# Performance work log

Measured on AMD Instinct MI355X. Metric: run time of the kernel, lower is better.

## Reference

```python
import jax, jax.numpy as jnp
import numpy as np

B, S, H = 2, 2048, 2048
NH = 16
Q_LORA = 1536
KV_LORA = 512
NOPE = 128
ROPE = 64
QHD = NOPE + ROPE  # 192
VHD = 128
FF = 8192
EPS = 1e-6
THETA = 10000.0


def rmsnorm(x, w, eps=EPS):
    var = jnp.mean(jnp.square(x), axis=-1, keepdims=True)
    return w * (x * jax.lax.rsqrt(var + eps))


def rotate_half(x):
    x1 = x[..., : x.shape[-1] // 2]
    x2 = x[..., x.shape[-1] // 2 :]
    return jnp.concatenate((-x2, x1), axis=-1)


def _deinterleave(x):
    # torch: x.view(b,h,s,d//2,2).transpose(0,1,2,4,3).reshape(b,h,s,d)
    b, h, s, d = x.shape
    return x.reshape(b, h, s, d // 2, 2).transpose(0, 1, 2, 4, 3).reshape(b, h, s, d)


def setup_inputs() -> dict:
    key = jax.random.key(0)
    ks = jax.random.split(key, 16)
    sc = 0.02
    # RoPE tables [S, ROPE]
    inv_freq = 1.0 / (THETA ** (np.arange(0, ROPE, 2, dtype=np.float64) / ROPE))
    freqs = np.outer(np.arange(S, dtype=np.float64), inv_freq)
    emb = np.concatenate([freqs, freqs], axis=-1)
    pos = jnp.sort(jax.random.randint(ks[15], (B, S), 0, S), axis=-1)
    return {
        "hidden_states": jax.random.normal(ks[0], (B, S, H), jnp.float32),
        "ln1_w": jnp.ones((H,), jnp.float32),
        "q_a_kernel": jax.random.normal(ks[1], (H, Q_LORA), jnp.float32) * sc,
        "q_a_ln_w": jnp.ones((Q_LORA,), jnp.float32),
        "q_b_kernel": jax.random.normal(ks[2], (Q_LORA, NH * QHD), jnp.float32) * sc,
        "kv_a_kernel": jax.random.normal(ks[3], (H, KV_LORA + ROPE), jnp.float32) * sc,
        "kv_a_ln_w": jnp.ones((KV_LORA,), jnp.float32),
        "kv_b_kernel": jax.random.normal(ks[4], (KV_LORA, NH * (NOPE + VHD)), jnp.float32) * sc,
        "o_kernel": jax.random.normal(ks[5], (NH * VHD, H), jnp.float32) * sc,
        "ln2_w": jnp.ones((H,), jnp.float32),
        "gate_kernel": jax.random.normal(ks[6], (H, FF), jnp.float32) * sc,
        "up_kernel": jax.random.normal(ks[7], (H, FF), jnp.float32) * sc,
        "down_kernel": jax.random.normal(ks[8], (FF, H), jnp.float32) * sc,
        "sin": jnp.asarray(np.sin(emb), jnp.float32),
        "cos": jnp.asarray(np.cos(emb), jnp.float32),
        "position_ids": pos,
    }


def reference(hidden_states, ln1_w, q_a_kernel, q_a_ln_w, q_b_kernel,
              kv_a_kernel, kv_a_ln_w, kv_b_kernel, o_kernel, ln2_w,
              gate_kernel, up_kernel, down_kernel, sin, cos, position_ids):
    b, s, h = hidden_states.shape
    x = rmsnorm(hidden_states, ln1_w)

    # --- MLA attention ---
    q = rmsnorm(x @ q_a_kernel, q_a_ln_w) @ q_b_kernel        # [b,s,NH*QHD]
    q = q.reshape(b, s, NH, QHD).transpose(0, 2, 1, 3)        # [b,NH,s,QHD]
    q_nope, q_pe = q[..., :NOPE], q[..., NOPE:]

    ckv = x @ kv_a_kernel                                     # [b,s,KV_LORA+ROPE]
    k_pe = ckv[..., KV_LORA:].reshape(b, s, 1, ROPE).transpose(0, 2, 1, 3)  # [b,1,s,ROPE]
    kv = rmsnorm(ckv[..., :KV_LORA], kv_a_ln_w) @ kv_b_kernel
    kv = kv.reshape(b, s, NH, NOPE + VHD).transpose(0, 2, 1, 3)
    k_nope = kv[..., :NOPE]
    v = kv[..., NOPE:]                                        # [b,NH,s,VHD]

    cos_e = cos[position_ids][:, None]                        # [b,1,s,ROPE]
    sin_e = sin[position_ids][:, None]
    q_pe = _deinterleave(q_pe)
    k_pe = _deinterleave(k_pe)
    q_pe = q_pe * cos_e + rotate_half(q_pe) * sin_e
    k_pe = k_pe * cos_e + rotate_half(k_pe) * sin_e

    qs = jnp.concatenate([q_nope, q_pe], axis=-1)             # [b,NH,s,QHD]
    ks = jnp.concatenate([k_nope, jnp.broadcast_to(k_pe, (b, NH, s, ROPE))], axis=-1)

    scale = QHD ** -0.5
    scores = jnp.einsum("bhqd,bhkd->bhqk", qs, ks) * scale
    causal = jnp.tril(jnp.ones((s, s), dtype=bool))
    scores = jnp.where(causal, scores, jnp.finfo(scores.dtype).min)
    probs = jax.nn.softmax(scores, axis=-1)
    attn = jnp.einsum("bhqk,bhkd->bhqd", probs, v)            # [b,NH,s,VHD]
    attn = attn.transpose(0, 2, 1, 3).reshape(b, s, NH * VHD)
    attn_out = attn @ o_kernel

    h1 = hidden_states + attn_out

    # --- dense MLP (SwiGLU) ---
    x2 = rmsnorm(h1, ln2_w)
    mlp = (jax.nn.silu(x2 @ gate_kernel) * (x2 @ up_kernel)) @ down_kernel
    return h1 + mlp
```

## Files before the change

### kernel.cpp

```cpp
#include <hip/hip_runtime.h>
#include <hip/hip_bf16.h>
#include <cstdint>

#define B_ 2
#define S_ 2048
#define H_ 2048
#define NH_ 16
#define QL_ 1536
#define KVL_ 512
#define NOPE_ 128
#define ROPE_ 64
#define QHD_ 192
#define VHD_ 128
#define FF_ 8192
#define BS_ (B_ * S_)
#define CKVP_ 640
#define KVW_ (NOPE_ + VHD_)

typedef __hip_bfloat16 bf16;
typedef __attribute__((ext_vector_type(8))) short short8_t;
typedef __attribute__((ext_vector_type(4))) float f32x4;

__device__ __forceinline__ float ldf(const float* p, size_t i) { return p[i]; }
__device__ __forceinline__ float ldf(const bf16* p, size_t i) { return __bfloat162float(p[i]); }
__device__ __forceinline__ void stf(float* p, size_t i, float v) { p[i] = v; }
__device__ __forceinline__ void stf(bf16* p, size_t i, float v) { p[i] = __float2bfloat16(v); }

__device__ __forceinline__ void gload16(const void* g, void* l)
{
    __builtin_amdgcn_global_load_lds((const unsigned int*)g, (unsigned int*)l, 16, 0, 0);
}

__global__ __launch_bounds__(256) void transp_bf16(
    const float* __restrict__ in, bf16* __restrict__ out, int K, int N, int Npad)
{
    __shared__ float t[32][33];
    const int n0 = blockIdx.x * 32, k0 = blockIdx.y * 32;
    for (int r = threadIdx.y; r < 32; r += 8) {
        const int n = n0 + threadIdx.x;
        t[r][threadIdx.x] = (n < N) ? in[(size_t)(k0 + r) * N + n] : 0.f;
    }
    __syncthreads();
    for (int r = threadIdx.y; r < 32; r += 8) {
        out[(size_t)(n0 + r) * K + k0 + threadIdx.x] = __float2bfloat16(t[threadIdx.x][r]);
    }
}

template<typename InT, typename OutT>
__global__ __launch_bounds__(256) void rmsnorm2(
    const InT* __restrict__ in, const float* __restrict__ w,
    OutT* __restrict__ out, int cols, int istride, int ostride)
{
    const int row = blockIdx.x;
    const InT* ip = in + (size_t)row * istride;
    OutT* op = out + (size_t)row * ostride;

    float ss = 0.f;
    for (int c = threadIdx.x; c < cols; c += 256) {
        float v = ldf(ip, c);
        ss = fmaf(v, v, ss);
    }
    #pragma unroll
    for (int off = 32; off; off >>= 1) ss += __shfl_xor(ss, off);
    __shared__ float red[4];
    if ((threadIdx.x & 63) == 0) red[threadIdx.x >> 6] = ss;
    __syncthreads();
    const float total = red[0] + red[1] + red[2] + red[3];
    const float scale = rsqrtf(total / (float)cols + 1e-6f);
    for (int c = threadIdx.x; c < cols; c += 256) {
        stf(op, c, ldf(ip, c) * scale * w[c]);
    }
}

template<int MODE, typename OutT>
__global__ __launch_bounds__(256) void gemm_bf16(
    const bf16* __restrict__ A, const bf16* __restrict__ BT,
    const float* __restrict__ Df, const bf16* __restrict__ Db,
    OutT* __restrict__ C, int M, int N, int K)
{
    __shared__ short As[128 * 32];
    __shared__ short Bs[128 * 32];
    const int tid = threadIdx.x;
    const int wid = tid >> 6, lane = tid & 63;
    const int bm = blockIdx.y * 128, bn = blockIdx.x * 128;
    const int wr = (wid >> 1) * 64, wc = (wid & 1) * 64;
    const int l16 = lane & 15;
    const int lk = (lane >> 4) << 3;

    f32x4 acc[4][4] = {};

    for (int k0 = 0; k0 < K; k0 += 32) {
        #pragma unroll
        for (int is = 0; is < 2; ++is) {
            const int c = is * 256 + tid;
            const int row = c >> 2;
            const int cb = (c & 3) * 16;
            const char* srcA = (const char*)A + ((size_t)(bm + row) * K + k0) * 2 + cb;
            const char* srcB = (const char*)BT + ((size_t)(bn + row) * K + k0) * 2 + cb;
            char* dstA = (char*)As + (is * 256 + wid * 64) * 16;
            char* dstB = (char*)Bs + (is * 256 + wid * 64) * 16;
            gload16(srcA, dstA);
            gload16(srcB, dstB);
        }
        __syncthreads();

        short8_t a[4], b[4];
        const short* ApW = As + (wr + l16) * 32 + lk;
        const short* BpW = Bs + (wc + l16) * 32 + lk;
        #pragma unroll
        for (int m = 0; m < 4; ++m) a[m] = *(const short8_t*)(ApW + m * 16 * 32);
        #pragma unroll
        for (int n = 0; n < 4; ++n) b[n] = *(const short8_t*)(BpW + n * 16 * 32);
        #pragma unroll
        for (int m = 0; m < 4; ++m)
            #pragma unroll
            for (int n = 0; n < 4; ++n)
                acc[m][n] = __builtin_amdgcn_mfma_f32_16x16x32_bf16(a[m], b[n], acc[m][n], 0, 0, 0);
        __syncthreads();
    }

    const int r0 = bm + wr + ((lane >> 4) << 2);
    const int c0 = bn + wc + l16;
    #pragma unroll
    for (int m = 0; m < 4; ++m) {
        #pragma unroll
        for (int n = 0; n < 4; ++n) {
            const int row = r0 + m * 16;
            const int col = c0 + n * 16;
            #pragma unroll
            for (int r = 0; r < 4; ++r) {
                const size_t off = (size_t)(row + r) * N + col;
                float v = acc[m][n][r];
                if (MODE == 1) v += Df[off];
                if (MODE == 2) {
                    const float g = __bfloat162float(Db[off]);
                    v *= g / (1.f + __expf(-g));
                }
                stf(C, off, v);
            }
        }
    }
}

template<int MODE, typename OutT>
__device__ __forceinline__ void epi_store(
    OutT* __restrict__ C, const float* __restrict__ Df, const bf16* __restrict__ Db,
    int N, int row, int col, float v)
{
    const size_t off = (size_t)row * N + col;
    if (MODE == 1) v += Df[off];
    if (MODE == 2) {
        const float g = __bfloat162float(Db[off]);
        v *= g / (1.f + __expf(-g));
    }
    stf(C, off, v);
}

__device__ __forceinline__ short8_t ldsfrag(const short* half_base, int r, int c)
{
    return *(const short8_t*)(half_base + r * 64 + ((c ^ (r & 7)) << 3));
}

template<int MODE, typename OutT>
__global__ __launch_bounds__(512, 2) void gemm256(
    const bf16* __restrict__ A, const bf16* __restrict__ BT,
    const float* __restrict__ Df, const bf16* __restrict__ Db,
    OutT* __restrict__ C, int M, int N, int K)
{
    __shared__ short lds[2][2][2][128 * 64];

    const int tid = threadIdx.x;
    const int wid = tid >> 6, lane = tid & 63;
    const int wm = wid >> 2, wn = wid & 3;
    const int l16 = lane & 15, hk = lane >> 4;

    const int nwg = gridDim.x * gridDim.y;
    const int orig = blockIdx.y * gridDim.x + blockIdx.x;
    const int q = nwg >> 3, r8 = nwg & 7;
    const int xcd = orig & 7, lid = orig >> 3;
    const int wg = (xcd < r8 ? xcd * (q + 1) : r8 * (q + 1) + (xcd - r8) * q) + lid;
    const int bn = (wg % gridDim.x) * 256;
    const int bm = (wg / gridDim.x) * 256;

    f32x4 acc[8][4] = {};
    const int nt = K >> 6;

    auto stage_half = [&](const bf16* gbase, short* lbase) {
        #pragma unroll
        for (int i = 0; i < 2; ++i) {
            const int ch = i * 512 + tid;
            const int row = ch >> 3, pc = ch & 7;
            const int gc = pc ^ (row & 7);
            const char* src = (const char*)(gbase + (size_t)row * K + gc * 8);
            char* dst = (char*)lbase + (i * 512 + wid * 64) * 16;
            gload16(src, dst);
        }
    };
    auto stage_tile = [&](int t, int buf) {
        const int k0 = t << 6;
        stage_half(A + (size_t)bm * K + k0,          &lds[buf][0][0][0]);
        stage_half(A + (size_t)(bm + 128) * K + k0,  &lds[buf][0][1][0]);
        stage_half(BT + (size_t)bn * K + k0,         &lds[buf][1][0][0]);
        stage_half(BT + (size_t)(bn + 128) * K + k0, &lds[buf][1][1][0]);
    };

    stage_tile(0, 0);
    stage_tile(1, 1);
    asm volatile("s_waitcnt vmcnt(8)" ::: "memory");
    __builtin_amdgcn_s_barrier();

    int cur = 0;
    for (int t = 0; t < nt; ++t) {
        const short* Ah = &lds[cur][0][wm][0];
        const short* Bh = &lds[cur][1][wn >> 1][0];
        const int brr = (wn & 1) * 64;

        short8_t bfr[4][2], afr[2][2];

        #pragma unroll
        for (int nf = 0; nf < 4; ++nf)
            #pragma unroll
            for (int ks = 0; ks < 2; ++ks)
                bfr[nf][ks] = ldsfrag(Bh, brr + nf * 16 + l16, ks * 4 + hk);
        #pragma unroll
        for (int mi = 0; mi < 2; ++mi)
            #pragma unroll
            for (int ks = 0; ks < 2; ++ks)
                afr[mi][ks] = ldsfrag(Ah, mi * 16 + l16, ks * 4 + hk);
        __builtin_amdgcn_s_barrier();
        __builtin_amdgcn_s_setprio(1);
        #pragma unroll
        for (int mi = 0; mi < 2; ++mi)
            #pragma unroll
            for (int nf = 0; nf < 4; ++nf)
                #pragma unroll
                for (int ks = 0; ks < 2; ++ks)
                    acc[mi][nf] = __builtin_amdgcn_mfma_f32_16x16x32_bf16(
                        afr[mi][ks], bfr[nf][ks], acc[mi][nf], 0, 0, 0);
        __builtin_amdgcn_s_setprio(0);
        __builtin_amdgcn_s_barrier();

        #pragma unroll
        for (int ph = 1; ph < 4; ++ph) {
            #pragma unroll
            for (int mi = 0; mi < 2; ++mi)
                #pragma unroll
                for (int ks = 0; ks < 2; ++ks)
                    afr[mi][ks] = ldsfrag(Ah, ph * 32 + mi * 16 + l16, ks * 4 + hk);
            __builtin_amdgcn_s_barrier();
            __builtin_amdgcn_s_setprio(1);
            #pragma unroll
            for (int mi = 0; mi < 2; ++mi)
                #pragma unroll
                for (int nf = 0; nf < 4; ++nf)
                    #pragma unroll
                    for (int ks = 0; ks < 2; ++ks)
                        acc[ph * 2 + mi][nf] = __builtin_amdgcn_mfma_f32_16x16x32_bf16(
                            afr[mi][ks], bfr[nf][ks], acc[ph * 2 + mi][nf], 0, 0, 0);
            __builtin_amdgcn_s_setprio(0);
            __builtin_amdgcn_s_barrier();
        }

        if (t + 2 < nt) {
            stage_tile(t + 2, cur);
            asm volatile("s_waitcnt vmcnt(8)" ::: "memory");
        } else if (t + 1 < nt) {
            asm volatile("s_waitcnt vmcnt(0)" ::: "memory");
        }
        __builtin_amdgcn_s_barrier();
        cur ^= 1;
    }

    const int r0 = bm + wm * 128 + (lane >> 4) * 4;
    const int c0 = bn + wn * 64 + l16;
    #pragma unroll
    for (int mf = 0; mf < 8; ++mf)
        #pragma unroll
        for (int nf = 0; nf < 4; ++nf)
            #pragma unroll
            for (int r = 0; r < 4; ++r)
                epi_store<MODE>(C, Df, Db, N, r0 + mf * 16 + r, c0 + nf * 16, acc[mf][nf][r]);
}

template<int MODE, typename OutT>
__global__ __launch_bounds__(512, 2) void gemm256n128(
    const bf16* __restrict__ A, const bf16* __restrict__ BT,
    const float* __restrict__ Df, const bf16* __restrict__ Db,
    OutT* __restrict__ C, int M, int N, int K)
{
    __shared__ short lds[2][3][128 * 64];

    const int tid = threadIdx.x;
    const int wid = tid >> 6, lane = tid & 63;
    const int wm = wid >> 1, wn = wid & 1;
    const int l16 = lane & 15, hk = lane >> 4;

    const int nwg = gridDim.x * gridDim.y;
    const int orig = blockIdx.y * gridDim.x + blockIdx.x;
    const int q = nwg >> 3, r8 = nwg & 7;
    const int xcd = orig & 7, lid = orig >> 3;
    const int wg = (xcd < r8 ? xcd * (q + 1) : r8 * (q + 1) + (xcd - r8) * q) + lid;
    const int bn = (wg % gridDim.x) * 128;
    const int bm = (wg / gridDim.x) * 256;

    f32x4 acc[4][4] = {};
    const int nt = K >> 6;

    auto stage_half = [&](const bf16* gbase, short* lbase) {
        #pragma unroll
        for (int i = 0; i < 2; ++i) {
            const int ch = i * 512 + tid;
            const int row = ch >> 3, pc = ch & 7;
            const int gc = pc ^ (row & 7);
            const char* src = (const char*)(gbase + (size_t)row * K + gc * 8);
            char* dst = (char*)lbase + (i * 512 + wid * 64) * 16;
            gload16(src, dst);
        }
    };
    auto stage_tile = [&](int t, int buf) {
        const int k0 = t << 6;
        stage_half(A + (size_t)bm * K + k0,          &lds[buf][0][0]);
        stage_half(A + (size_t)(bm + 128) * K + k0,  &lds[buf][1][0]);
        stage_half(BT + (size_t)bn * K + k0,         &lds[buf][2][0]);
    };

    stage_tile(0, 0);
    stage_tile(1, 1);
    asm volatile("s_waitcnt vmcnt(6)" ::: "memory");
    __builtin_amdgcn_s_barrier();

    int cur = 0;
    for (int t = 0; t < nt; ++t) {
        const short* Ah = &lds[cur][wm >> 1][0];
        const short* Bh = &lds[cur][2][0];
        const int arr = (wm & 1) * 64;
        const int brr = wn * 64;

        short8_t bfr[4][2], afr[2][2];

        #pragma unroll
        for (int nf = 0; nf < 4; ++nf)
            #pragma unroll
            for (int ks = 0; ks < 2; ++ks)
                bfr[nf][ks] = ldsfrag(Bh, brr + nf * 16 + l16, ks * 4 + hk);
        #pragma unroll
        for (int mi = 0; mi < 2; ++mi)
            #pragma unroll
            for (int ks = 0; ks < 2; ++ks)
                afr[mi][ks] = ldsfrag(Ah, arr + mi * 16 + l16, ks * 4 + hk);
        __builtin_amdgcn_s_barrier();
        __builtin_amdgcn_s_setprio(1);
        #pragma unroll
        for (int mi = 0; mi < 2; ++mi)
            #pragma unroll
            for (int nf = 0; nf < 4; ++nf)
                #pragma unroll
                for (int ks = 0; ks < 2; ++ks)
                    acc[mi][nf] = __builtin_amdgcn_mfma_f32_16x16x32_bf16(
                        afr[mi][ks], bfr[nf][ks], acc[mi][nf], 0, 0, 0);
        __builtin_amdgcn_s_setprio(0);
        __builtin_amdgcn_s_barrier();

        #pragma unroll
        for (int mi = 0; mi < 2; ++mi)
            #pragma unroll
            for (int ks = 0; ks < 2; ++ks)
                afr[mi][ks] = ldsfrag(Ah, arr + 32 + mi * 16 + l16, ks * 4 + hk);
        __builtin_amdgcn_s_barrier();
        __builtin_amdgcn_s_setprio(1);
        #pragma unroll
        for (int mi = 0; mi < 2; ++mi)
            #pragma unroll
            for (int nf = 0; nf < 4; ++nf)
                #pragma unroll
                for (int ks = 0; ks < 2; ++ks)
                    acc[2 + mi][nf] = __builtin_amdgcn_mfma_f32_16x16x32_bf16(
                        afr[mi][ks], bfr[nf][ks], acc[2 + mi][nf], 0, 0, 0);
        __builtin_amdgcn_s_setprio(0);
        __builtin_amdgcn_s_barrier();

        if (t + 2 < nt) {
            stage_tile(t + 2, cur);
            asm volatile("s_waitcnt vmcnt(6)" ::: "memory");
        } else if (t + 1 < nt) {
            asm volatile("s_waitcnt vmcnt(0)" ::: "memory");
        }
        __builtin_amdgcn_s_barrier();
        cur ^= 1;
    }

    const int r0 = bm + wm * 64 + (lane >> 4) * 4;
    const int c0 = bn + wn * 64 + l16;
    #pragma unroll
    for (int mf = 0; mf < 4; ++mf)
        #pragma unroll
        for (int nf = 0; nf < 4; ++nf)
            #pragma unroll
            for (int r = 0; r < 4; ++r)
                epi_store<MODE>(C, Df, Db, N, r0 + mf * 16 + r, c0 + nf * 16, acc[mf][nf][r]);
}

__global__ __launch_bounds__(256) void rope_kernel(
    bf16* __restrict__ q, float* __restrict__ ckv,
    const int* __restrict__ pos_ids,
    const float* __restrict__ sinT, const float* __restrict__ cosT)
{
    const int wid = blockIdx.x * 4 + (threadIdx.x >> 6);
    const int lane = threadIdx.x & 63;
    const int NQ = BS_ * NH_;

    int bs;
    bf16* bptr = nullptr;
    float* fptr = nullptr;
    if (wid < NQ) {
        bs = wid >> 4;
        bptr = q + (size_t)wid * QHD_ + NOPE_;
    } else {
        bs = wid - NQ;
        fptr = ckv + (size_t)bs * CKVP_ + KVL_;
    }
    const int pos = pos_ids[bs];
    const float c  = cosT[pos * ROPE_ + lane];
    const float sn = sinT[pos * ROPE_ + lane];
    const float x = bptr ? __bfloat162float(bptr[lane]) : fptr[lane];
    const int j = lane & 31;
    const float x0 = __shfl(x, 2 * j);
    const float x1 = __shfl(x, 2 * j + 1);
    const float res = (lane < 32) ? fmaf(x0, c, -x1 * sn) : fmaf(x1, c, x0 * sn);
    if (bptr) bptr[lane] = __float2bfloat16(res);
    else      fptr[lane] = res;
}

__global__ __launch_bounds__(256) void pack_k(
    const float* __restrict__ KV, const float* __restrict__ CKV,
    bf16* __restrict__ Kh)
{
    const int total = BS_ * NH_ * (QHD_ / 2);
    for (int i = blockIdx.x * 256 + threadIdx.x; i < total; i += gridDim.x * 256) {
        const int d2 = i % (QHD_ / 2);
        const int t  = i / (QHD_ / 2);
        const int s  = t % S_;
        const int hh = (t / S_) % NH_;
        const int bb = t / (S_ * NH_);
        const int d = d2 * 2;
        float2 v;
        if (d < NOPE_) v = *(const float2*)&KV[(((size_t)bb * S_ + s) * NH_ + hh) * KVW_ + d];
        else           v = *(const float2*)&CKV[((size_t)bb * S_ + s) * CKVP_ + KVL_ + (d - NOPE_)];
        union { bf16 h[2]; unsigned int u; } cv;
        cv.h[0] = __float2bfloat16(v.x);
        cv.h[1] = __float2bfloat16(v.y);
        *(unsigned int*)&Kh[((size_t)(bb * NH_ + hh) * S_ + s) * QHD_ + d] = cv.u;
    }
}

__global__ __launch_bounds__(256) void pack_vt(
    const float* __restrict__ KV, bf16* __restrict__ Vt)
{
    __shared__ float t[32][33];
    const int s0 = blockIdx.x * 32, d0 = blockIdx.y * 32;
    const int bh = blockIdx.z;
    const int tx = threadIdx.x & 31, ty = threadIdx.x >> 5;
    for (int r = ty; r < 32; r += 8)
        t[r][tx] = KV[(((size_t)(bh >> 4) * S_ + s0 + r) * NH_ + (bh & 15)) * KVW_ + NOPE_ + d0 + tx];
    __syncthreads();
    for (int r = ty; r < 32; r += 8)
        Vt[((size_t)bh * VHD_ + d0 + r) * S_ + s0 + tx] = __float2bfloat16(t[tx][r]);
}

__global__ __launch_bounds__(512, 2) void attn_mfma(
    const bf16* __restrict__ Qp, const bf16* __restrict__ Kh,
    const bf16* __restrict__ Vt, bf16* __restrict__ outp)
{
    __shared__ __align__(16) short Ks[64][192];
    __shared__ __align__(16) short Vs[128][64];
    __shared__ __align__(16) short Ps[8][16][64];

    const int tid = threadIdx.x;
    const int wid = tid >> 6, lane = tid & 63;
    const int l16 = lane & 15;
    const int hk  = lane >> 4;
    const int lk  = hk << 3;
    const int pr  = hk << 2;
    const int lx  = l16 & 7;

    const int bid = blockIdx.x;
    const int orig = (bid & 7) * 64 + (bid >> 3);
    const int j  = orig & 15;
    const int gh = orig >> 4;
    const int h = gh & 15, b = gh >> 4;

    const int setB = wid >> 2;
    const int qblk = setB ? (31 - j) : j;
    const int qw = qblk * 64 + (wid & 3) * 16;
    const int myNt = qblk + 1;
    const int ntStage = 32 - j;

    short8_t qf[6];
    const bf16* qbase = Qp + (((size_t)b * S_ + qw + l16) * NH_ + h) * QHD_;
    #pragma unroll
    for (int kk = 0; kk < 6; ++kk)
        qf[kk] = *(const short8_t*)(qbase + kk * 32 + lk);

    const bf16* Khb = Kh + (size_t)(b * NH_ + h) * S_ * QHD_;
    const bf16* Vtb = Vt + (size_t)(b * NH_ + h) * VHD_ * S_;

    f32x4 o[8] = {};
    float mr[4] = {-3.0e38f, -3.0e38f, -3.0e38f, -3.0e38f};
    float lr[4] = {0.f, 0.f, 0.f, 0.f};
    const float scale = 0.07216878364870323f;

    const int krow = tid >> 3, kc0 = (tid & 7) * 3;
    const int vrow = tid >> 2, vc0 = (tid & 3) * 2;

    short8_t kreg[3], vreg[2];
    auto load_tile = [&](int kt) {
        const short* ksrc = (const short*)(Khb + ((size_t)(kt * 64 + krow)) * QHD_);
        kreg[0] = *(const short8_t*)(ksrc + (kc0 + 0) * 8);
        kreg[1] = *(const short8_t*)(ksrc + (kc0 + 1) * 8);
        kreg[2] = *(const short8_t*)(ksrc + (kc0 + 2) * 8);
        const short* vsrc = (const short*)(Vtb + (size_t)vrow * S_ + kt * 64);
        vreg[0] = *(const short8_t*)(vsrc + (vc0 + 0) * 8);
        vreg[1] = *(const short8_t*)(vsrc + (vc0 + 1) * 8);
    };
    auto write_tile = [&]() {
        const int kx = krow & 7, vx = vrow & 7;
        *(short8_t*)&Ks[krow][((kc0 + 0) ^ kx) << 3] = kreg[0];
        *(short8_t*)&Ks[krow][((kc0 + 1) ^ kx) << 3] = kreg[1];
        *(short8_t*)&Ks[krow][((kc0 + 2) ^ kx) << 3] = kreg[2];
        *(short8_t*)&Vs[vrow][((vc0 + 0) ^ vx) << 3] = vreg[0];
        *(short8_t*)&Vs[vrow][((vc0 + 1) ^ vx) << 3] = vreg[1];
    };

    load_tile(0);

    for (int t = 0; t < ntStage; ++t) {
        write_tile();
        __syncthreads();
        if (t + 1 < ntStage) load_tile(t + 1);
        if (t < myNt) {
            const int k0 = t << 6;
            f32x4 s[4] = {};
            #pragma unroll
            for (int kk = 0; kk < 6; ++kk) {
                #pragma unroll
                for (int n = 0; n < 4; ++n) {
                    short8_t kf = *(const short8_t*)&Ks[n * 16 + l16][((kk * 4 + hk) ^ lx) << 3];
                    s[n] = __builtin_amdgcn_mfma_f32_16x16x32_bf16(qf[kk], kf, s[n], 0, 0, 0);
                }
            }
            if (t == myNt - 1) {
                #pragma unroll
                for (int n = 0; n < 4; ++n) {
                    const int kg = k0 + n * 16 + l16;
                    #pragma unroll
                    for (int r = 0; r < 4; ++r) {
                        if (kg > qw + pr + r) s[n][r] = -3.0e38f;
                    }
                }
            }
            #pragma unroll
            for (int r = 0; r < 4; ++r) {
                float rm = fmaxf(fmaxf(s[0][r], s[1][r]), fmaxf(s[2][r], s[3][r]));
                rm = fmaxf(rm, __shfl_xor(rm, 1));
                rm = fmaxf(rm, __shfl_xor(rm, 2));
                rm = fmaxf(rm, __shfl_xor(rm, 4));
                rm = fmaxf(rm, __shfl_xor(rm, 8));
                const float mnew = fmaxf(mr[r], rm);
                const float corr = __expf((mr[r] - mnew) * scale);
                mr[r] = mnew;
                float rs = 0.f;
                #pragma unroll
                for (int n = 0; n < 4; ++n) {
                    const float p = __expf((s[n][r] - mnew) * scale);
                    s[n][r] = p;
                    rs += p;
                }
                rs += __shfl_xor(rs, 1);
                rs += __shfl_xor(rs, 2);
                rs += __shfl_xor(rs, 4);
                rs += __shfl_xor(rs, 8);
                lr[r] = lr[r] * corr + rs;
                #pragma unroll
                for (int n = 0; n < 8; ++n) o[n][r] *= corr;
            }
            #pragma unroll
            for (int n = 0; n < 4; ++n) {
                #pragma unroll
                for (int r = 0; r < 4; ++r) {
                    union { bf16 hh; short u; } cv;
                    cv.hh = __float2bfloat16(s[n][r]);
                    const int row = pr + r;
                    const int col = (((n * 2 + (l16 >> 3)) ^ (row & 7)) << 3) + (l16 & 7);
                    Ps[wid][row][col] = cv.u;
                }
            }
            #pragma unroll
            for (int kk2 = 0; kk2 < 2; ++kk2) {
                short8_t pf = *(const short8_t*)&Ps[wid][l16][((kk2 * 4 + hk) ^ lx) << 3];
                #pragma unroll
                for (int n = 0; n < 8; ++n) {
                    short8_t vf = *(const short8_t*)&Vs[n * 16 + l16][((kk2 * 4 + hk) ^ lx) << 3];
                    o[n] = __builtin_amdgcn_mfma_f32_16x16x32_bf16(pf, vf, o[n], 0, 0, 0);
                }
            }
        }
        __syncthreads();
    }

    float inv[4];
    #pragma unroll
    for (int r = 0; r < 4; ++r) inv[r] = 1.f / lr[r];
    bf16* ob = outp + (((size_t)b * S_ + qw + pr) * NH_ + h) * VHD_;
    #pragma unroll
    for (int r = 0; r < 4; ++r)
        #pragma unroll
        for (int n = 0; n < 8; ++n)
            ob[(size_t)r * (NH_ * VHD_) + n * 16 + l16] = __float2bfloat16(o[n][r] * inv[r]);
}

extern "C" void kernel_launch(void* const* d_in, const int* in_sizes, int n_in,
                              void* d_out, int out_size, void* d_ws, size_t ws_size,
                              hipStream_t stream)
{
    const float* hidden  = (const float*)d_in[0];
    const float* ln1_w   = (const float*)d_in[1];
    const float* q_a_k   = (const float*)d_in[2];
    const float* q_a_ln  = (const float*)d_in[3];
    const float* q_b_k   = (const float*)d_in[4];
    const float* kv_a_k  = (const float*)d_in[5];
    const float* kv_a_ln = (const float*)d_in[6];
    const float* kv_b_k  = (const float*)d_in[7];
    const float* o_k     = (const float*)d_in[8];
    const float* ln2_w   = (const float*)d_in[9];
    const float* gate_k  = (const float*)d_in[10];
    const float* up_k    = (const float*)d_in[11];
    const float* down_k  = (const float*)d_in[12];
    const float* sinT    = (const float*)d_in[13];
    const float* cosT    = (const float*)d_in[14];
    const int*   pos     = (const int*)d_in[15];
    float* out = (float*)d_out;
    char* ws = (char*)d_ws;

    bf16* qaT   = (bf16*)(ws + 0);
    bf16* qbT   = (bf16*)(ws + 6291456);
    bf16* kvaT  = (bf16*)(ws + 15728640);
    bf16* kvbT  = (bf16*)(ws + 18350080);
    bf16* oT    = (bf16*)(ws + 22544384);
    bf16* Xb    = (bf16*)(ws + 30932992);
    bf16* QAb   = (bf16*)(ws + 47710208);
    bf16* CKVNb = (bf16*)(ws + 60293120);
    bf16* Qb    = (bf16*)(ws + 64487424);
    float* CKV  = (float*)(ws + 89653248);
    float* KV   = (float*)(ws + 100139008);
    bf16* ATTNb = (bf16*)(ws + 167247872);
    bf16* Vt    = (bf16*)(ws + 0);
    bf16* Kh    = (bf16*)(ws + 30932992);
    bf16* gateT = (bf16*)(ws + 0);
    bf16* upT   = (bf16*)(ws + 33554432);
    bf16* downT = (bf16*)(ws + 67108864);
    bf16* X2b   = (bf16*)(ws + 100663296);
    bf16* MLPb  = (bf16*)(ws + 117440512);

    const dim3 tb(32, 8);

    transp_bf16<<<dim3(1536 / 32, 2048 / 32), tb, 0, stream>>>(q_a_k, qaT, 2048, 1536, 1536);
    transp_bf16<<<dim3(3072 / 32, 1536 / 32), tb, 0, stream>>>(q_b_k, qbT, 1536, 3072, 3072);
    transp_bf16<<<dim3(640 / 32, 2048 / 32), tb, 0, stream>>>(kv_a_k, kvaT, 2048, 576, 640);
    transp_bf16<<<dim3(4096 / 32, 512 / 32), tb, 0, stream>>>(kv_b_k, kvbT, 512, 4096, 4096);
    transp_bf16<<<dim3(2048 / 32, 2048 / 32), tb, 0, stream>>>(o_k, oT, 2048, 2048, 2048);

    rmsnorm2<float, bf16><<<BS_, 256, 0, stream>>>(hidden, ln1_w, Xb, H_, H_, H_);
    gemm_bf16<0, bf16><<<dim3(QL_ / 128, BS_ / 128), 256, 0, stream>>>(
        Xb, qaT, nullptr, nullptr, QAb, BS_, QL_, H_);
    rmsnorm2<bf16, bf16><<<BS_, 256, 0, stream>>>(QAb, q_a_ln, QAb, QL_, QL_, QL_);
    gemm256n128<0, bf16><<<dim3((NH_ * QHD_) / 128, BS_ / 256), 512, 0, stream>>>(
        QAb, qbT, nullptr, nullptr, Qb, BS_, NH_ * QHD_, QL_);
    gemm_bf16<0, float><<<dim3(CKVP_ / 128, BS_ / 128), 256, 0, stream>>>(
        Xb, kvaT, nullptr, nullptr, CKV, BS_, CKVP_, H_);
    rmsnorm2<float, bf16><<<BS_, 256, 0, stream>>>(CKV, kv_a_ln, CKVNb, KVL_, CKVP_, KVL_);
    gemm256<0, float><<<dim3((NH_ * KVW_) / 256, BS_ / 256), 512, 0, stream>>>(
        CKVNb, kvbT, nullptr, nullptr, KV, BS_, NH_ * KVW_, KVL_);
    rope_kernel<<<(BS_ * NH_ + BS_) / 4, 256, 0, stream>>>(Qb, CKV, pos, sinT, cosT);
    pack_k<<<2048, 256, 0, stream>>>(KV, CKV, Kh);
    pack_vt<<<dim3(S_ / 32, VHD_ / 32, B_ * NH_), 256, 0, stream>>>(KV, Vt);
    attn_mfma<<<dim3(512), 512, 0, stream>>>(Qb, Kh, Vt, ATTNb);
    gemm256n128<1, float><<<dim3(H_ / 128, BS_ / 256), 512, 0, stream>>>(
        ATTNb, oT, hidden, nullptr, out, BS_, H_, NH_ * VHD_);

    transp_bf16<<<dim3(8192 / 32, 2048 / 32), tb, 0, stream>>>(gate_k, gateT, 2048, 8192, 8192);
    transp_bf16<<<dim3(8192 / 32, 2048 / 32), tb, 0, stream>>>(up_k, upT, 2048, 8192, 8192);
    transp_bf16<<<dim3(2048 / 32, 8192 / 32), tb, 0, stream>>>(down_k, downT, 8192, 2048, 2048);

    rmsnorm2<float, bf16><<<BS_, 256, 0, stream>>>(out, ln2_w, X2b, H_, H_, H_);
    gemm256<0, bf16><<<dim3(FF_ / 256, BS_ / 256), 512, 0, stream>>>(
        X2b, gateT, nullptr, nullptr, MLPb, BS_, FF_, H_);
    gemm256<2, bf16><<<dim3(FF_ / 256, BS_ / 256), 512, 0, stream>>>(
        X2b, upT, nullptr, MLPb, MLPb, BS_, FF_, H_);
    gemm256n128<1, float><<<dim3(H_ / 128, BS_ / 256), 512, 0, stream>>>(
        MLPb, downT, out, nullptr, out, BS_, H_, FF_);
}
```

Before: 1.004 ms.

## Fuse gate and up GEMMs into one dual-B kernel with SiLU epilogue

```diff
diff --git a/kernel.cpp b/kernel.cpp
--- a/kernel.cpp
+++ b/kernel.cpp
@@ -218,30 +218,14 @@
         short8_t bfr[4][2], afr[2][2];
 
         #pragma unroll
-        for (int nf = 0; nf < 4; ++nf)
-            #pragma unroll
-            for (int ks = 0; ks < 2; ++ks)
-                bfr[nf][ks] = ldsfrag(Bh, brr + nf * 16 + l16, ks * 4 + hk);
-        #pragma unroll
-        for (int mi = 0; mi < 2; ++mi)
-            #pragma unroll
-            for (int ks = 0; ks < 2; ++ks)
-                afr[mi][ks] = ldsfrag(Ah, mi * 16 + l16, ks * 4 + hk);
-        __builtin_amdgcn_s_barrier();
-        __builtin_amdgcn_s_setprio(1);
-        #pragma unroll
-        for (int mi = 0; mi < 2; ++mi)
-            #pragma unroll
-            for (int nf = 0; nf < 4; ++nf)
-                #pragma unroll
-                for (int ks = 0; ks < 2; ++ks)
-                    acc[mi][nf] = __builtin_amdgcn_mfma_f32_16x16x32_bf16(
-                        afr[mi][ks], bfr[nf][ks], acc[mi][nf], 0, 0, 0);
-        __builtin_amdgcn_s_setprio(0);
-        __builtin_amdgcn_s_barrier();
-
-        #pragma unroll
-        for (int ph = 1; ph < 4; ++ph) {
+        for (int ph = 0; ph < 4; ++ph) {
+            if (ph == 0) {
+                #pragma unroll
+                for (int nf = 0; nf < 4; ++nf)
+                    #pragma unroll
+                    for (int ks = 0; ks < 2; ++ks)
+                        bfr[nf][ks] = ldsfrag(Bh, brr + nf * 16 + l16, ks * 4 + hk);
+            }
             #pragma unroll
             for (int mi = 0; mi < 2; ++mi)
                 #pragma unroll
@@ -258,9 +242,9 @@
                         acc[ph * 2 + mi][nf] = __builtin_amdgcn_mfma_f32_16x16x32_bf16(
                             afr[mi][ks], bfr[nf][ks], acc[ph * 2 + mi][nf], 0, 0, 0);
             __builtin_amdgcn_s_setprio(0);
-            __builtin_amdgcn_s_barrier();
-        }
-
+        }
+
+        __builtin_amdgcn_s_barrier();
         if (t + 2 < nt) {
             stage_tile(t + 2, cur);
             asm volatile("s_waitcnt vmcnt(8)" ::: "memory");
@@ -339,46 +323,33 @@
         short8_t bfr[4][2], afr[2][2];
 
         #pragma unroll
-        for (int nf = 0; nf < 4; ++nf)
-            #pragma unroll
-            for (int ks = 0; ks < 2; ++ks)
-                bfr[nf][ks] = ldsfrag(Bh, brr + nf * 16 + l16, ks * 4 + hk);
-        #pragma unroll
-        for (int mi = 0; mi < 2; ++mi)
-            #pragma unroll
-            for (int ks = 0; ks < 2; ++ks)
-                afr[mi][ks] = ldsfrag(Ah, arr + mi * 16 + l16, ks * 4 + hk);
+        for (int ph = 0; ph < 2; ++ph) {
+            if (ph == 0) {
+                #pragma unroll
+                for (int nf = 0; nf < 4; ++nf)
+                    #pragma unroll
+                    for (int ks = 0; ks < 2; ++ks)
+                        bfr[nf][ks] = ldsfrag(Bh, brr + nf * 16 + l16, ks * 4 + hk);
+            }
+            #pragma unroll
+            for (int mi = 0; mi < 2; ++mi)
+                #pragma unroll
+                for (int ks = 0; ks < 2; ++ks)
+                    afr[mi][ks] = ldsfrag(Ah, arr + ph * 32 + mi * 16 + l16, ks * 4 + hk);
+            __builtin_amdgcn_s_barrier();
+            __builtin_amdgcn_s_setprio(1);
+            #pragma unroll
+            for (int mi = 0; mi < 2; ++mi)
+                #pragma unroll
+                for (int nf = 0; nf < 4; ++nf)
+                    #pragma unroll
+                    for (int ks = 0; ks < 2; ++ks)
+                        acc[ph * 2 + mi][nf] = __builtin_amdgcn_mfma_f32_16x16x32_bf16(
+                            afr[mi][ks], bfr[nf][ks], acc[ph * 2 + mi][nf], 0, 0, 0);
+            __builtin_amdgcn_s_setprio(0);
+        }
+
         __builtin_amdgcn_s_barrier();
-        __builtin_amdgcn_s_setprio(1);
-        #pragma unroll
-        for (int mi = 0; mi < 2; ++mi)
-            #pragma unroll
-            for (int nf = 0; nf < 4; ++nf)
-                #pragma unroll
-                for (int ks = 0; ks < 2; ++ks)
-                    acc[mi][nf] = __builtin_amdgcn_mfma_f32_16x16x32_bf16(
-                        afr[mi][ks], bfr[nf][ks], acc[mi][nf], 0, 0, 0);
-        __builtin_amdgcn_s_setprio(0);
-        __builtin_amdgcn_s_barrier();
-
-        #pragma unroll
-        for (int mi = 0; mi < 2; ++mi)
-            #pragma unroll
-            for (int ks = 0; ks < 2; ++ks)
-                afr[mi][ks] = ldsfrag(Ah, arr + 32 + mi * 16 + l16, ks * 4 + hk);
-        __builtin_amdgcn_s_barrier();
-        __builtin_amdgcn_s_setprio(1);
-        #pragma unroll
-        for (int mi = 0; mi < 2; ++mi)
-            #pragma unroll
-            for (int nf = 0; nf < 4; ++nf)
-                #pragma unroll
-                for (int ks = 0; ks < 2; ++ks)
-                    acc[2 + mi][nf] = __builtin_amdgcn_mfma_f32_16x16x32_bf16(
-                        afr[mi][ks], bfr[nf][ks], acc[2 + mi][nf], 0, 0, 0);
-        __builtin_amdgcn_s_setprio(0);
-        __builtin_amdgcn_s_barrier();
-
         if (t + 2 < nt) {
             stage_tile(t + 2, cur);
             asm volatile("s_waitcnt vmcnt(6)" ::: "memory");
@@ -398,6 +369,120 @@
             #pragma unroll
             for (int r = 0; r < 4; ++r)
                 epi_store<MODE>(C, Df, Db, N, r0 + mf * 16 + r, c0 + nf * 16, acc[mf][nf][r]);
+}
+
+__global__ __launch_bounds__(512, 2) void gemm256dual(
+    const bf16* __restrict__ A, const bf16* __restrict__ BG,
+    const bf16* __restrict__ BU, bf16* __restrict__ C, int M, int N, int K)
+{
+    __shared__ short lds[2][4][128 * 64];
+
+    const int tid = threadIdx.x;
+    const int wid = tid >> 6, lane = tid & 63;
+    const int wm = wid >> 1, wn = wid & 1;
+    const int l16 = lane & 15, hk = lane >> 4;
+
+    const int nwg = gridDim.x * gridDim.y;
+    const int orig = blockIdx.y * gridDim.x + blockIdx.x;
+    const int q = nwg >> 3, r8 = nwg & 7;
+    const int xcd = orig & 7, lid = orig >> 3;
+    const int wg = (xcd < r8 ? xcd * (q + 1) : r8 * (q + 1) + (xcd - r8) * q) + lid;
+    const int bm = (wg % gridDim.y) * 256;
+    const int bn = (wg / gridDim.y) * 128;
+
+    f32x4 g[4][4] = {}, u[4][4] = {};
+    const int nt = K >> 6;
+
+    auto stage_half = [&](const bf16* gbase, short* lbase) {
+        #pragma unroll
+        for (int i = 0; i < 2; ++i) {
+            const int ch = i * 512 + tid;
+            const int row = ch >> 3, pc = ch & 7;
+            const int gc = pc ^ (row & 7);
+            const char* src = (const char*)(gbase + (size_t)row * K + gc * 8);
+            char* dst = (char*)lbase + (i * 512 + wid * 64) * 16;
+            gload16(src, dst);
+        }
+    };
+    auto stage_tile = [&](int t, int buf) {
+        const int k0 = t << 6;
+        stage_half(A + (size_t)bm * K + k0,          &lds[buf][0][0]);
+        stage_half(A + (size_t)(bm + 128) * K + k0,  &lds[buf][1][0]);
+        stage_half(BG + (size_t)bn * K + k0,         &lds[buf][2][0]);
+        stage_half(BU + (size_t)bn * K + k0,         &lds[buf][3][0]);
+    };
+
+    stage_tile(0, 0);
+    stage_tile(1, 1);
+    asm volatile("s_waitcnt vmcnt(8)" ::: "memory");
+    __builtin_amdgcn_s_barrier();
+
+    int cur = 0;
+    for (int t = 0; t < nt; ++t) {
+        const short* Ah = &lds[cur][wm >> 1][0];
+        const short* Gh = &lds[cur][2][0];
+        const short* Uh = &lds[cur][3][0];
+        const int arr = (wm & 1) * 64;
+        const int brr = wn * 64;
+
+        short8_t gfr[4][2], ufr[4][2], afr[2][2];
+
+        #pragma unroll
+        for (int ph = 0; ph < 2; ++ph) {
+            if (ph == 0) {
+                #pragma unroll
+                for (int nf = 0; nf < 4; ++nf)
+                    #pragma unroll
+                    for (int ks = 0; ks < 2; ++ks) {
+                        gfr[nf][ks] = ldsfrag(Gh, brr + nf * 16 + l16, ks * 4 + hk);
+                        ufr[nf][ks] = ldsfrag(Uh, brr + nf * 16 + l16, ks * 4 + hk);
+                    }
+            }
+            #pragma unroll
+            for (int mi = 0; mi < 2; ++mi)
+                #pragma unroll
+                for (int ks = 0; ks < 2; ++ks)
+                    afr[mi][ks] = ldsfrag(Ah, arr + ph * 32 + mi * 16 + l16, ks * 4 + hk);
+            __builtin_amdgcn_s_barrier();
+            __builtin_amdgcn_s_setprio(1);
+            #pragma unroll
+            for (int mi = 0; mi < 2; ++mi)
+                #pragma unroll
+                for (int nf = 0; nf < 4; ++nf)
+                    #pragma unroll
+                    for (int ks = 0; ks < 2; ++ks) {
+                        g[ph * 2 + mi][nf] = __builtin_amdgcn_mfma_f32_16x16x32_bf16(
+                            afr[mi][ks], gfr[nf][ks], g[ph * 2 + mi][nf], 0, 0, 0);
+                        u[ph * 2 + mi][nf] = __builtin_amdgcn_mfma_f32_16x16x32_bf16(
+                            afr[mi][ks], ufr[nf][ks], u[ph * 2 + mi][nf], 0, 0, 0);
+                    }
+            __builtin_amdgcn_s_setprio(0);
+        }
+
+        __builtin_amdgcn_s_barrier();
+        if (t + 2 < nt) {
+            stage_tile(t + 2, cur);
+            asm volatile("s_waitcnt vmcnt(8)" ::: "memory");
+        } else if (t + 1 < nt) {
+            asm volatile("s_waitcnt vmcnt(0)" ::: "memory");
+        }
+        __builtin_amdgcn_s_barrier();
+        cur ^= 1;
+    }
+
+    const int r0 = bm + wm * 64 + (lane >> 4) * 4;
+    const int c0 = bn + wn * 64 + l16;
+    #pragma unroll
+    for (int mf = 0; mf < 4; ++mf)
+        #pragma unroll
+        for (int nf = 0; nf < 4; ++nf)
+            #pragma unroll
+            for (int r = 0; r < 4; ++r) {
+                const float gg = g[mf][nf][r];
+                const float uu = u[mf][nf][r];
+                const float v = gg / (1.f + __expf(-gg)) * uu;
+                C[(size_t)(r0 + mf * 16 + r) * N + c0 + nf * 16] = __float2bfloat16(v);
+            }
 }
 
 __global__ __launch_bounds__(256) void rope_kernel(
@@ -692,10 +777,8 @@
     transp_bf16<<<dim3(2048 / 32, 8192 / 32), tb, 0, stream>>>(down_k, downT, 8192, 2048, 2048);
 
     rmsnorm2<float, bf16><<<BS_, 256, 0, stream>>>(out, ln2_w, X2b, H_, H_, H_);
-    gemm256<0, bf16><<<dim3(FF_ / 256, BS_ / 256), 512, 0, stream>>>(
-        X2b, gateT, nullptr, nullptr, MLPb, BS_, FF_, H_);
-    gemm256<2, bf16><<<dim3(FF_ / 256, BS_ / 256), 512, 0, stream>>>(
-        X2b, upT, nullptr, MLPb, MLPb, BS_, FF_, H_);
+    gemm256dual<<<dim3(FF_ / 128, BS_ / 256), 512, 0, stream>>>(
+        X2b, gateT, upT, MLPb, BS_, FF_, H_);
     gemm256n128<1, float><<<dim3(H_ / 128, BS_ / 256), 512, 0, stream>>>(
         MLPb, downT, out, nullptr, out, BS_, H_, FF_);
 }
```

After: 973.4 us. 1.03x faster.
